# Performance work log

Measured on AMD Instinct MI355X. Metric: run time of the kernel, lower is better.

## Reference

```python
import jax, jax.numpy as jnp
import numpy as np

R, MAXI, MAXO = 333, 119, 12   # n ROIs, max roi input size, max roi reduced size
E, H = 3328, 8                  # embed dim (concat 3325 + pad 3), heads
HD = E // H                     # 416
CONCAT = 3325
EPS = 1e-5


def _roi_layout():
    """Deterministic synthetic ROI sizes + gather maps for vectorized ragged encode."""
    sizes = 30 + (7 * np.arange(R)) % 90            # per-ROI input widths
    reduced = 8 + np.arange(R) % 5                  # per-ROI output widths
    reduced[332] = 8                                # makes concat+3 divisible by 8
    starts = np.concatenate([[0], np.cumsum(sizes)[:-1]])
    total = int(sizes.sum())                        # 24696
    in_idx = np.minimum(starts[:, None] + np.arange(MAXI)[None, :], total - 1)
    in_mask = (np.arange(MAXI)[None, :] < sizes[:, None]).astype(np.float32)
    out_idx = np.concatenate([i * MAXO + np.arange(reduced[i]) for i in range(R)])
    assert out_idx.shape[0] == CONCAT
    return jnp.asarray(in_idx), jnp.asarray(in_mask), jnp.asarray(out_idx)


def _bn(x, g, b):
    # training-mode BatchNorm1d: biased batch stats (matches torch normalization)
    m = x.mean(0)
    v = x.var(0)
    return (x - m) * jax.lax.rsqrt(v + EPS) * g + b


def _lrelu(x, s):
    return jnp.where(x > 0, x, s * x)


def setup_inputs() -> dict:
    key = jax.random.key(0)
    ks = jax.random.split(key, 16)
    B, TOTAL = 2048, 24696
    f32 = jnp.float32
    return {
        'x': jax.random.normal(ks[0], (B, TOTAL), f32),
        'enc_W': jax.random.normal(ks[1], (R, MAXO, MAXI), f32) * 0.1,
        'enc_b': jax.random.normal(ks[2], (R, MAXO), f32) * 0.02,
        'bn1_g': jnp.ones((CONCAT,), f32),
        'bn1_b': jnp.zeros((CONCAT,), f32),
        'Wqkv': jax.random.normal(ks[3], (3 * E, E), f32) * (1.0 / np.sqrt(E)),
        'bqkv': jnp.zeros((3 * E,), f32),
        'Wo': jax.random.normal(ks[4], (E, E), f32) * (1.0 / np.sqrt(E)),
        'bo': jnp.zeros((E,), f32),
        'W1': jax.random.normal(ks[5], (1024, E), f32) * (1.0 / np.sqrt(E)),
        'b1': jnp.zeros((1024,), f32),
        'bn2_g': jnp.ones((1024,), f32),
        'bn2_b': jnp.zeros((1024,), f32),
        'W2': jax.random.normal(ks[6], (300, 1024), f32) * (1.0 / 32.0),
        'b2': jnp.zeros((300,), f32),
        'Wc': jax.random.normal(ks[7], (180, 300), f32) * 0.06,
        'bc': jnp.zeros((180,), f32),
    }


def reference(x, enc_W, enc_b, bn1_g, bn1_b, Wqkv, bqkv, Wo, bo,
              W1, b1, bn2_g, bn2_b, W2, b2, Wc, bc):
    in_idx, in_mask, out_idx = _roi_layout()
    B = x.shape[0]
    # --- vectorized ragged per-ROI Linear (replaces 333-way python loop) ---
    xp = x[:, in_idx] * in_mask                     # [B, R, MAXI], padded slices
    y = jnp.einsum('bri,roi->bro', xp, enc_W) + enc_b  # [B, R, MAXO]
    y = y.reshape(B, R * MAXO)[:, out_idx]          # ragged concat -> [B, 3325]
    # per-ROI BN+LeakyReLU(0.3) == per-feature on the concat
    y = _lrelu(_bn(y, bn1_g, bn1_b), 0.3)
    y = jnp.pad(y, ((0, 0), (1, 2)))                # F.pad (1, 2) -> [B, 3328]
    # --- MultiheadAttention, seq_len = 1 (input unsqueezed to [1, B, E]) ---
    qkv = y @ Wqkv.T + bqkv                         # [B, 3E]
    q, k, v = jnp.split(qkv, 3, axis=-1)
    q = q.reshape(B, H, 1, HD)
    k = k.reshape(B, H, 1, HD)
    v = v.reshape(B, H, 1, HD)
    s = jnp.einsum('bhqd,bhkd->bhqk', q, k) / jnp.sqrt(jnp.float32(HD))
    a = jax.nn.softmax(s, axis=-1)                  # trivially 1 for L=1, kept faithful
    o = jnp.einsum('bhqk,bhkd->bhqd', a, v).reshape(B, E)
    o = o @ Wo.T + bo
    r = _lrelu(_bn(o @ W1.T + b1, bn2_g, bn2_b), 0.1)
    reg_out = r @ W2.T + b2                         # [B, 300]
    y_pred = jax.nn.softmax(reg_out @ Wc.T + bc, axis=-1)  # [B, 180]
    return reg_out, y_pred
```

## Files before the change

kernel.cpp:

```cpp
#include <hip/hip_runtime.h>
#include <hip/hip_bf16.h>

#define B_      2048
#define R_      333
#define MAXI_   119
#define MAXO_   12
#define CONCAT_ 3325
#define E_      3328
#define TOTAL_  24696
#define HID_    1024
#define NREG_   300
#define NCLS_   180
#define EPS_    1e-5f
#define NS2_    128

typedef __attribute__((ext_vector_type(8))) short bf16x8;
typedef __attribute__((ext_vector_type(4))) float f32x4;

static __device__ inline unsigned short f2bf_rne(float f) {
  unsigned u;
  __builtin_memcpy(&u, &f, 4);
  u += 0x7fff + ((u >> 16) & 1);
  return (unsigned short)(u >> 16);
}
static __device__ inline float bf2f(unsigned short s) {
  unsigned u = (unsigned)s << 16;
  float f;
  __builtin_memcpy(&f, &u, 4);
  return f;
}

__global__ void layout_kernel(int* __restrict__ starts, int* __restrict__ red_starts) {
  if (threadIdx.x == 0 && blockIdx.x == 0) {
    int s = 0, rs = 0;
    for (int r = 0; r < R_; ++r) {
      starts[r] = s;
      red_starts[r] = rs;
      s += 30 + (7 * r) % 90;
      rs += (r == 332) ? 8 : (8 + r % 5);
    }
  }
}

__device__ __forceinline__ void rowdot_body(
    const float* __restrict__ A, const float* __restrict__ v, const float* __restrict__ b,
    float* __restrict__ out, int N, int K, int jb) {
  int wid = threadIdx.x >> 6, lane = threadIdx.x & 63;
  int j = jb * 4 + wid;
  if (j >= N) return;
  const float* row = A + (size_t)j * K;
  float s = 0.f;
  for (int k = lane; k < K; k += 64) s = fmaf(row[k], v[k], s);
  for (int o = 32; o; o >>= 1) s += __shfl_down(s, o);
  if (lane == 0) out[j] = s + b[j];
}

__device__ __forceinline__ void pack_w_body(const float* __restrict__ enc_W,
                                            const int* __restrict__ starts,
                                            unsigned short* __restrict__ Wpk, int r) {
  int tid = threadIdx.x;
  int kc = tid >> 6, lane = tid & 63;
  int size = 30 + (7 * r) % 90;
  int s8 = starts[r] & 7;
  int oc = lane & 15;
  int k0 = kc * 32 + (lane >> 4) * 8;
  unsigned short o[8];
#pragma unroll
  for (int e = 0; e < 8; ++e) {
    int k = k0 + e - s8;
    float v = 0.f;
    if (oc < MAXO_ && k >= 0 && k < size) v = enc_W[((size_t)r * MAXO_ + oc) * MAXI_ + k];
    o[e] = f2bf_rne(v);
  }
  unsigned short* dst = Wpk + ((size_t)r * 4 + kc) * 512 + lane * 8;
  *(ushort4*)dst = *(ushort4*)&o[0];
  *(ushort4*)(dst + 4) = *(ushort4*)&o[4];
}

#define NTR_    ((E_ / 64) * (E_ / 64))
#define NC4A_   (HID_ * E_ / 4)
#define NC4B_   (NREG_ * HID_ / 4)
#define NCAST_  ((NC4A_ + NC4B_ + 255) / 256)
__global__ __launch_bounds__(256) void prep_kernel(
    const float* __restrict__ Wo, const float* __restrict__ Wv,
    unsigned short* __restrict__ WoT, unsigned short* __restrict__ WvT,
    const float* __restrict__ W1, unsigned short* __restrict__ W1b,
    const float* __restrict__ W2, unsigned short* __restrict__ W2b,
    const float* __restrict__ bv, const float* __restrict__ bo, float* __restrict__ t1v,
    const float* __restrict__ enc_W, const int* __restrict__ starts,
    unsigned short* __restrict__ Wpk) {
  __shared__ float tile[64][65];
  int bid = blockIdx.x;
  if (bid < 2 * NTR_) {
    int z = bid / NTR_, rem = bid % NTR_;
    const float* in = z ? Wv : Wo;
    unsigned short* out = z ? WvT : WoT;
    int c0 = (rem % 52) * 64, r0 = (rem / 52) * 64;
    int t = threadIdx.x;
    int ci = t & 63, ri0 = t >> 6;
    for (int ri = ri0; ri < 64; ri += 4)
      tile[ri][ci] = in[(size_t)(r0 + ri) * E_ + c0 + ci];
    __syncthreads();
    int rj = t & 63, i0 = t >> 6;
    for (int i = i0; i < 64; i += 4)
      out[(size_t)(c0 + i) * E_ + r0 + rj] = f2bf_rne(tile[rj][i]);
  } else if (bid < 2 * NTR_ + NCAST_) {
    int i = (bid - 2 * NTR_) * 256 + threadIdx.x;
    const float* src; unsigned short* dst; int idx;
    if (i < NC4A_) { src = W1; dst = W1b; idx = i; }
    else if (i < NC4A_ + NC4B_) { src = W2; dst = W2b; idx = i - NC4A_; }
    else return;
    float4 v = ((const float4*)src)[idx];
    ushort4 o;
    o.x = f2bf_rne(v.x); o.y = f2bf_rne(v.y); o.z = f2bf_rne(v.z); o.w = f2bf_rne(v.w);
    ((ushort4*)dst)[idx] = o;
  } else if (bid < 2 * NTR_ + NCAST_ + E_ / 4) {
    rowdot_body(Wo, bv, bo, t1v, E_, E_, bid - 2 * NTR_ - NCAST_);
  } else {
    pack_w_body(enc_W, starts, Wpk, bid - 2 * NTR_ - NCAST_ - E_ / 4);
  }
}

__device__ __forceinline__ void encode_body(
    const float* __restrict__ x, const unsigned short* __restrict__ Wpk,
    const float* __restrict__ enc_b, const int* __restrict__ starts,
    const int* __restrict__ red_starts,
    unsigned short* __restrict__ yT, int r, int bg) {
  int tid = threadIdx.x;
  int wid = tid >> 6, lane = tid & 63;
  int lr = lane & 15, kg = lane >> 4;

  int size = 30 + (7 * r) % 90;
  int red  = (r == 332) ? 8 : (8 + r % 5);
  int st   = starts[r];
  int s8   = st & 7;
  int a0   = st & ~7;
  int rs   = red_starts[r];
  int nkc  = (s8 + size + 31) >> 5;
  int kmax = TOTAL_ - a0;

  bf16x8 wf[4];
  const unsigned short* wp = Wpk + (size_t)r * 2048 + lane * 8;
#pragma unroll
  for (int kc = 0; kc < 4; ++kc) wf[kc] = *(const bf16x8*)(wp + kc * 512);

  float bofs[4];
#pragma unroll
  for (int reg = 0; reg < 4; ++reg) {
    int oc = kg * 4 + reg;
    bofs[reg] = (oc < MAXO_) ? enc_b[r * MAXO_ + oc] : 0.f;
  }

  for (int t = 0; t < 4; ++t) {
    int b0 = bg * 256 + wid * 64 + t * 16;
    const float* xrow = x + (size_t)(b0 + lr) * TOTAL_ + a0;
    f32x4 acc = {0.f, 0.f, 0.f, 0.f};
#pragma unroll
    for (int kc = 0; kc < 4; ++kc) {
      if (kc < nkc) {
        int k0 = kc * 32 + kg * 8;
        if (k0 + 8 > kmax) k0 = kmax - 8;
        float4 v0 = *(const float4*)(xrow + k0);
        float4 v1 = *(const float4*)(xrow + k0 + 4);
        bf16x8 xf;
        xf[0] = (short)f2bf_rne(v0.x); xf[1] = (short)f2bf_rne(v0.y);
        xf[2] = (short)f2bf_rne(v0.z); xf[3] = (short)f2bf_rne(v0.w);
        xf[4] = (short)f2bf_rne(v1.x); xf[5] = (short)f2bf_rne(v1.y);
        xf[6] = (short)f2bf_rne(v1.z); xf[7] = (short)f2bf_rne(v1.w);
        acc = __builtin_amdgcn_mfma_f32_16x16x32_bf16(wf[kc], xf, acc, 0, 0, 0);
      }
    }
#pragma unroll
    for (int reg = 0; reg < 4; ++reg) {
      int oc = kg * 4 + reg;
      if (oc < red)
        yT[(size_t)(rs + oc) * B_ + b0 + lr] = f2bf_rne(acc[reg] + bofs[reg]);
    }
  }
}

template <int KS, bool OUT_BF16>
__device__ __forceinline__ void gemm_body(
    const unsigned short* __restrict__ A, const unsigned short* __restrict__ W,
    float* __restrict__ Cf, unsigned short* __restrict__ Cb,
    int M, int N, int K, int bx, int by, int bz, unsigned short* smem) {
  unsigned short* a_lds = smem;
  unsigned short* b_lds = smem + 8192;
  int tid = threadIdx.x;
  int wid = tid >> 6, lane = tid & 63;
  int wr = wid >> 1, wc = wid & 1;
  int row0 = by * 128, col0 = bx * 128;
  int lr = lane & 15, kg = lane >> 4;
  int Klocal = K / KS;
  int kbase = bz * Klocal;

  int srow = tid >> 2, sk = (tid & 3) * 8;
  const unsigned short* aptr0 = A + (size_t)(row0 + srow) * K + kbase + sk;
  const unsigned short* aptr1 = aptr0 + (size_t)64 * K;
  int bcol0 = col0 + srow;      if (bcol0 > N - 1) bcol0 = N - 1;
  int bcol1 = col0 + 64 + srow; if (bcol1 > N - 1) bcol1 = N - 1;
  const unsigned short* bptr0 = W + (size_t)bcol0 * K + kbase + sk;
  const unsigned short* bptr1 = W + (size_t)bcol1 * K + kbase + sk;

  f32x4 acc[4][4] = {};
  int nk = Klocal >> 5;

#define STAGE_(buf, kc)                                                                             \
  do {                                                                                              \
    __builtin_amdgcn_global_load_lds((const __attribute__((address_space(1))) void*)(aptr0 + (kc)), \
        (__attribute__((address_space(3))) void*)(a_lds + (buf) * 4096 + wid * 512), 16, 0, 0);     \
    __builtin_amdgcn_global_load_lds((const __attribute__((address_space(1))) void*)(aptr1 + (kc)), \
        (__attribute__((address_space(3))) void*)(a_lds + (buf) * 4096 + 2048 + wid * 512), 16, 0, 0); \
    __builtin_amdgcn_global_load_lds((const __attribute__((address_space(1))) void*)(bptr0 + (kc)), \
        (__attribute__((address_space(3))) void*)(b_lds + (buf) * 4096 + wid * 512), 16, 0, 0);     \
    __builtin_amdgcn_global_load_lds((const __attribute__((address_space(1))) void*)(bptr1 + (kc)), \
        (__attribute__((address_space(3))) void*)(b_lds + (buf) * 4096 + 2048 + wid * 512), 16, 0, 0); \
  } while (0)

  STAGE_(0, 0);
  __syncthreads();
  int cur = 0;
  for (int t = 0; t < nk; ++t) {
    if (t + 1 < nk) STAGE_(cur ^ 1, (t + 1) * 32);
    bf16x8 a[4], b[4];
#pragma unroll
    for (int f = 0; f < 4; ++f) {
      a[f] = *(const bf16x8*)(a_lds + cur * 4096 + (wr * 64 + f * 16 + lr) * 32 + kg * 8);
      b[f] = *(const bf16x8*)(b_lds + cur * 4096 + (wc * 64 + f * 16 + lr) * 32 + kg * 8);
    }
#pragma unroll
    for (int i = 0; i < 4; ++i)
#pragma unroll
      for (int j = 0; j < 4; ++j)
        acc[i][j] = __builtin_amdgcn_mfma_f32_16x16x32_bf16(a[i], b[j], acc[i][j], 0, 0, 0);
    __syncthreads();
    cur ^= 1;
  }
#undef STAGE_

#pragma unroll
  for (int j = 0; j < 4; ++j) {
    int ccol = col0 + wc * 64 + j * 16 + lr;
    if (ccol >= N) continue;
#pragma unroll
    for (int i = 0; i < 4; ++i) {
#pragma unroll
      for (int reg = 0; reg < 4; ++reg) {
        int crow = row0 + wr * 64 + i * 16 + kg * 4 + reg;
        float v = acc[i][j][reg];
        if (KS == 1) {
          if (OUT_BF16) Cb[(size_t)crow * N + ccol] = f2bf_rne(v);
          else          Cf[(size_t)crow * N + ccol] = v;
        } else {
          Cf[((size_t)bz * M + crow) * N + ccol] = v;
        }
      }
    }
  }
}

#define WA_NB_  ((E_ / 128) * (HID_ / 128))
#define ENC_NB_ (R_ * 8)
__global__ __launch_bounds__(256) void mega_kernel(
    const float* __restrict__ x, const unsigned short* __restrict__ Wpk,
    const float* __restrict__ enc_b, const int* __restrict__ starts,
    const int* __restrict__ red_starts, unsigned short* __restrict__ yT,
    const unsigned short* __restrict__ W1b, const unsigned short* __restrict__ WoT,
    unsigned short* __restrict__ Wa_bf,
    const float* __restrict__ W1, const float* __restrict__ t1v,
    const float* __restrict__ b1, float* __restrict__ zbv) {
  __shared__ __align__(16) unsigned short smem[16384];
  int bid = blockIdx.x;
  if (bid < WA_NB_) {
    gemm_body<1, true>(W1b, WoT, nullptr, Wa_bf, HID_, E_, E_,
                       bid % (E_ / 128), bid / (E_ / 128), 0, smem);
  } else if (bid < WA_NB_ + ENC_NB_) {
    int eb = bid - WA_NB_;
    encode_body(x, Wpk, enc_b, starts, red_starts, yT, eb >> 3, eb & 7);
  } else {
    rowdot_body(W1, t1v, b1, zbv, HID_, E_, bid - WA_NB_ - ENC_NB_);
  }
}

#define WB2_NB_ (WA_NB_ * 2)
#define ST_NB_  ((CONCAT_ + 15) / 16)
__global__ __launch_bounds__(256) void wb_stats_kernel(
    const unsigned short* __restrict__ Wa_bf, const unsigned short* __restrict__ WvT,
    float* __restrict__ Cpart,
    const unsigned short* __restrict__ yT, float* __restrict__ mean, float* __restrict__ rstd) {
  __shared__ __align__(16) unsigned short smem[16384];
  int bid = blockIdx.x;
  if (bid < WB2_NB_) {
    int z = bid / WA_NB_, rem = bid % WA_NB_;
    gemm_body<2, false>(Wa_bf, WvT, Cpart, nullptr, HID_, E_, E_,
                        rem % (E_ / 128), rem / (E_ / 128), z, smem);
  } else {
    int tb = bid - WB2_NB_;
    int t = threadIdx.x;
    int f = tb * 16 + (t >> 4);
    int j = t & 15;
    if (f >= CONCAT_) return;
    const unsigned short* p = yT + (size_t)f * B_ + j * 128;
    float s = 0.f, s2 = 0.f;
#pragma unroll
    for (int i = 0; i < 16; ++i) {
      bf16x8 v = *(const bf16x8*)(p + i * 8);
#pragma unroll
      for (int e = 0; e < 8; ++e) {
        float xv = bf2f((unsigned short)v[e]);
        s += xv; s2 = fmaf(xv, xv, s2);
      }
    }
#pragma unroll
    for (int m = 1; m <= 8; m <<= 1) { s += __shfl_xor(s, m); s2 += __shfl_xor(s2, m); }
    if (j == 0) {
      float mm = s / B_;
      float var = s2 / B_ - mm * mm;
      mean[f] = mm;
      rstd[f] = rsqrtf(var + EPS_);
    }
  }
}

#define TR_NB_ ((E_ / 64) * (B_ / 64))
#define CWB_NB_ (HID_ * E_ / 4 / 256)
__global__ __launch_bounds__(256) void trans_comb_kernel(
    const unsigned short* __restrict__ yT, const float* __restrict__ mean,
    const float* __restrict__ rstd, const float* __restrict__ g,
    const float* __restrict__ bb, unsigned short* __restrict__ Y,
    const float* __restrict__ Cpart, unsigned short* __restrict__ Wb_bf) {
  __shared__ float tile[64][65];
  int bid = blockIdx.x;
  if (bid < TR_NB_) {
    int cc0 = (bid % 52) * 64, b0 = (bid / 52) * 64;
    int t = threadIdx.x;
    int bi = t & 63, ci0 = t >> 6;
    for (int ci = ci0; ci < 64; ci += 4) {
      int c = cc0 + ci - 1;
      float v = 0.f;
      if (c >= 0 && c < CONCAT_) {
        float f = bf2f(yT[(size_t)c * B_ + b0 + bi]);
        v = (f - mean[c]) * rstd[c] * g[c] + bb[c];
        v = v > 0.f ? v : 0.3f * v;
      }
      tile[ci][bi] = v;
    }
    __syncthreads();
    int cj = t & 63, bj0 = t >> 6;
    for (int bj = bj0; bj < 64; bj += 4)
      Y[(size_t)(b0 + bj) * E_ + cc0 + cj] = f2bf_rne(tile[cj][bj]);
  } else {
    int i4 = (bid - TR_NB_) * 256 + threadIdx.x;
    const int MN4 = HID_ * E_ / 4;
    if (i4 >= MN4) return;
    float4 a = ((const float4*)Cpart)[i4];
    float4 b = ((const float4*)(Cpart + (size_t)HID_ * E_))[i4];
    ushort4 o;
    o.x = f2bf_rne(a.x + b.x); o.y = f2bf_rne(a.y + b.y);
    o.z = f2bf_rne(a.z + b.z); o.w = f2bf_rne(a.w + b.w);
    ((ushort4*)Wb_bf)[i4] = o;
  }
}

template <int KS, bool OUT_BF16>
__global__ __launch_bounds__(256) void gemm_kernel(
    const unsigned short* __restrict__ A, const unsigned short* __restrict__ W,
    float* __restrict__ Cf, unsigned short* __restrict__ Cb, int M, int N, int K) {
  __shared__ __align__(16) unsigned short smem[16384];
  gemm_body<KS, OUT_BF16>(A, W, Cf, Cb, M, N, K, blockIdx.x, blockIdx.y, blockIdx.z, smem);
}

__global__ __launch_bounds__(256) void combZ_stats_kernel(
    const float* __restrict__ Cpart, const float* __restrict__ zb,
    float* __restrict__ Z, float* __restrict__ pS, float* __restrict__ pS2) {
  int c = blockIdx.x * 256 + threadIdx.x;
  int ry = blockIdx.y;
  float zbc = zb[c];
  float s1 = 0.f, s2 = 0.f;
  for (int r = ry * 16; r < ry * 16 + 16; ++r) {
    float v = zbc;
#pragma unroll
    for (int z = 0; z < 4; ++z) v += Cpart[((size_t)z * B_ + r) * HID_ + c];
    Z[(size_t)r * HID_ + c] = v;
    s1 += v; s2 = fmaf(v, v, s2);
  }
  pS[ry * HID_ + c] = s1;
  pS2[ry * HID_ + c] = s2;
}

__global__ __launch_bounds__(256) void colstats_final_kernel(
    const float* __restrict__ pS, const float* __restrict__ pS2,
    float* __restrict__ mean, float* __restrict__ rstd) {
  int c = blockIdx.x * 256 + threadIdx.x;
  if (c >= HID_) return;
  float s = 0.f, s2 = 0.f;
  for (int i = 0; i < NS2_; ++i) { s += pS[i * HID_ + c]; s2 += pS2[i * HID_ + c]; }
  float m = s / B_;
  float v = s2 / B_ - m * m;
  mean[c] = m;
  rstd[c] = rsqrtf(v + EPS_);
}

__global__ __launch_bounds__(256) void bn2_apply_kernel(
    const float* __restrict__ Z, const float* __restrict__ mean, const float* __restrict__ rstd,
    const float* __restrict__ g, const float* __restrict__ bb, unsigned short* __restrict__ R) {
  int i = blockIdx.x * 256 + threadIdx.x;
  int c = i & (HID_ - 1);
  float v = (Z[i] - mean[c]) * rstd[c] * g[c] + bb[c];
  v = v > 0.f ? v : 0.1f * v;
  R[i] = f2bf_rne(v);
}

__global__ __launch_bounds__(256) void classifier_kernel(
    const float* __restrict__ Cpart, const float* __restrict__ b2,
    const float* __restrict__ Wc, const float* __restrict__ bc,
    float* __restrict__ reg_out, float* __restrict__ ypred) {
  int b = blockIdx.x;
  __shared__ __align__(16) float rrow[NREG_];
  __shared__ float sl[256];
  int tid = threadIdx.x;
  for (int i = tid; i < NREG_; i += 256) {
    float s = b2[i];
#pragma unroll
    for (int z = 0; z < 4; ++z) s += Cpart[((size_t)z * B_ + b) * NREG_ + i];
    rrow[i] = s;
    reg_out[(size_t)b * NREG_ + i] = s;
  }
  __syncthreads();
  float s = -1e30f;
  if (tid < NCLS_) {
    const float* w = Wc + (size_t)tid * NREG_;
    float acc = 0.f;
    for (int k = 0; k < NREG_; k += 4) {
      float4 wv = *(const float4*)(w + k);
      float4 rv = *(const float4*)(&rrow[k]);
      acc = fmaf(wv.x, rv.x, acc); acc = fmaf(wv.y, rv.y, acc);
      acc = fmaf(wv.z, rv.z, acc); acc = fmaf(wv.w, rv.w, acc);
    }
    s = acc + bc[tid];
  }
  sl[tid] = s;
  __syncthreads();
  for (int o = 128; o > 0; o >>= 1) {
    if (tid < o) sl[tid] = fmaxf(sl[tid], sl[tid + o]);
    __syncthreads();
  }
  float mx = sl[0];
  __syncthreads();
  float e = (tid < NCLS_) ? __expf(s - mx) : 0.f;
  sl[tid] = e;
  __syncthreads();
  for (int o = 128; o > 0; o >>= 1) {
    if (tid < o) sl[tid] += sl[tid + o];
    __syncthreads();
  }
  if (tid < NCLS_) ypred[(size_t)b * NCLS_ + tid] = e / sl[0];
}

extern "C" void kernel_launch(void* const* d_in, const int* in_sizes, int n_in,
                              void* d_out, int out_size, void* d_ws, size_t ws_size,
                              hipStream_t stream) {
  const float* x     = (const float*)d_in[0];
  const float* enc_W = (const float*)d_in[1];
  const float* enc_b = (const float*)d_in[2];
  const float* bn1_g = (const float*)d_in[3];
  const float* bn1_b = (const float*)d_in[4];
  const float* Wqkv  = (const float*)d_in[5];
  const float* bqkv  = (const float*)d_in[6];
  const float* Wo    = (const float*)d_in[7];
  const float* bo    = (const float*)d_in[8];
  const float* W1    = (const float*)d_in[9];
  const float* b1    = (const float*)d_in[10];
  const float* bn2_g = (const float*)d_in[11];
  const float* bn2_b = (const float*)d_in[12];
  const float* W2    = (const float*)d_in[13];
  const float* b2    = (const float*)d_in[14];
  const float* Wc    = (const float*)d_in[15];
  const float* bc    = (const float*)d_in[16];

  char* ws = (char*)d_ws;
  size_t off = 0;
  auto alloc = [&](size_t bytes) -> void* {
    void* p = ws + off;
    off += (bytes + 255) & ~(size_t)255;
    return p;
  };

  unsigned short* yT     = (unsigned short*)alloc((size_t)CONCAT_ * B_ * 2);
  float*          mean1  = (float*)alloc(CONCAT_ * 4);
  float*          rstd1  = (float*)alloc(CONCAT_ * 4);
  unsigned short* Ybf    = (unsigned short*)alloc((size_t)B_ * E_ * 2);
  unsigned short* Rbf    = (unsigned short*)alloc((size_t)B_ * HID_ * 2);
  unsigned short* WoT_bf = (unsigned short*)alloc((size_t)E_ * E_ * 2);
  unsigned short* WvT_bf = (unsigned short*)alloc((size_t)E_ * E_ * 2);
  unsigned short* W1_bf  = (unsigned short*)alloc((size_t)HID_ * E_ * 2);
  unsigned short* W2_bf  = (unsigned short*)alloc((size_t)NREG_ * HID_ * 2);
  unsigned short* Wa_bf  = (unsigned short*)alloc((size_t)HID_ * E_ * 2);
  unsigned short* Wb_bf  = (unsigned short*)alloc((size_t)HID_ * E_ * 2);
  unsigned short* Wpk    = (unsigned short*)alloc((size_t)R_ * 2048 * 2);
  float*          Cpart  = (float*)alloc((size_t)4 * B_ * HID_ * 4);
  float*          t1v    = (float*)alloc(E_ * 4);
  float*          zbv    = (float*)alloc(HID_ * 4);
  float*          partS  = (float*)alloc((size_t)NS2_ * HID_ * 4);
  float*          partS2 = (float*)alloc((size_t)NS2_ * HID_ * 4);
  float*          mean2  = (float*)alloc(HID_ * 4);
  float*          rstd2  = (float*)alloc(HID_ * 4);
  int*            starts = (int*)alloc(R_ * 4);
  int*            redst  = (int*)alloc(R_ * 4);

  float* Z = (float*)yT;

  layout_kernel<<<1, 1, 0, stream>>>(starts, redst);
  prep_kernel<<<2 * NTR_ + NCAST_ + E_ / 4 + R_, 256, 0, stream>>>(
      Wo, Wqkv + (size_t)2 * E_ * E_, WoT_bf, WvT_bf,
      W1, W1_bf, W2, W2_bf, bqkv + 2 * E_, bo, t1v, enc_W, starts, Wpk);
  mega_kernel<<<WA_NB_ + ENC_NB_ + HID_ / 4, 256, 0, stream>>>(
      x, Wpk, enc_b, starts, redst, yT, W1_bf, WoT_bf, Wa_bf, W1, t1v, b1, zbv);
  wb_stats_kernel<<<WB2_NB_ + ST_NB_, 256, 0, stream>>>(
      Wa_bf, WvT_bf, Cpart, yT, mean1, rstd1);
  trans_comb_kernel<<<TR_NB_ + CWB_NB_, 256, 0, stream>>>(
      yT, mean1, rstd1, bn1_g, bn1_b, Ybf, Cpart, Wb_bf);
  gemm_kernel<4, false><<<dim3(HID_ / 128, B_ / 128, 4), 256, 0, stream>>>(
      Ybf, Wb_bf, Cpart, nullptr, B_, HID_, E_);
  combZ_stats_kernel<<<dim3(HID_ / 256, NS2_), 256, 0, stream>>>(Cpart, zbv, Z, partS, partS2);
  colstats_final_kernel<<<(HID_ + 255) / 256, 256, 0, stream>>>(partS, partS2, mean2, rstd2);
  bn2_apply_kernel<<<(B_ * HID_) / 256, 256, 0, stream>>>(Z, mean2, rstd2, bn2_g, bn2_b, Rbf);
  gemm_kernel<4, false><<<dim3((NREG_ + 127) / 128, B_ / 128, 4), 256, 0, stream>>>(
      Rbf, W2_bf, Cpart, nullptr, B_, NREG_, HID_);
  float* reg_out = (float*)d_out;
  classifier_kernel<<<B_, 256, 0, stream>>>(
      Cpart, b2, Wc, bc, reg_out, reg_out + (size_t)B_ * NREG_);
}
```

Baseline: 313.6 us.

## Split encode across two fused launches to balance GEMM and encode work

The ROI encode is split so that each block handles 64 batch rows instead of 256, with twice the block count. Half of the encode blocks run alongside the Wa GEMM in the first fused kernel and the other half alongside the Wb GEMM in the second. BN1 stats then move to a kernel with the Wb combine, and the BN1 transpose becomes its own kernel. This is meant to balance memory-bound encode with compute-bound GEMM blocks across launches, at the cost of one extra kernel launch.

```diff
diff --git a/kernel.cpp b/kernel.cpp
--- a/kernel.cpp
+++ b/kernel.cpp
@@ -151,31 +151,29 @@
     bofs[reg] = (oc < MAXO_) ? enc_b[r * MAXO_ + oc] : 0.f;
   }
 
-  for (int t = 0; t < 4; ++t) {
-    int b0 = bg * 256 + wid * 64 + t * 16;
-    const float* xrow = x + (size_t)(b0 + lr) * TOTAL_ + a0;
-    f32x4 acc = {0.f, 0.f, 0.f, 0.f};
-#pragma unroll
-    for (int kc = 0; kc < 4; ++kc) {
-      if (kc < nkc) {
-        int k0 = kc * 32 + kg * 8;
-        if (k0 + 8 > kmax) k0 = kmax - 8;
-        float4 v0 = *(const float4*)(xrow + k0);
-        float4 v1 = *(const float4*)(xrow + k0 + 4);
-        bf16x8 xf;
-        xf[0] = (short)f2bf_rne(v0.x); xf[1] = (short)f2bf_rne(v0.y);
-        xf[2] = (short)f2bf_rne(v0.z); xf[3] = (short)f2bf_rne(v0.w);
-        xf[4] = (short)f2bf_rne(v1.x); xf[5] = (short)f2bf_rne(v1.y);
-        xf[6] = (short)f2bf_rne(v1.z); xf[7] = (short)f2bf_rne(v1.w);
-        acc = __builtin_amdgcn_mfma_f32_16x16x32_bf16(wf[kc], xf, acc, 0, 0, 0);
-      }
-    }
-#pragma unroll
-    for (int reg = 0; reg < 4; ++reg) {
-      int oc = kg * 4 + reg;
-      if (oc < red)
-        yT[(size_t)(rs + oc) * B_ + b0 + lr] = f2bf_rne(acc[reg] + bofs[reg]);
-    }
+  int b0 = bg * 64 + wid * 16;
+  const float* xrow = x + (size_t)(b0 + lr) * TOTAL_ + a0;
+  f32x4 acc = {0.f, 0.f, 0.f, 0.f};
+#pragma unroll
+  for (int kc = 0; kc < 4; ++kc) {
+    if (kc < nkc) {
+      int k0 = kc * 32 + kg * 8;
+      if (k0 + 8 > kmax) k0 = kmax - 8;
+      float4 v0 = *(const float4*)(xrow + k0);
+      float4 v1 = *(const float4*)(xrow + k0 + 4);
+      bf16x8 xf;
+      xf[0] = (short)f2bf_rne(v0.x); xf[1] = (short)f2bf_rne(v0.y);
+      xf[2] = (short)f2bf_rne(v0.z); xf[3] = (short)f2bf_rne(v0.w);
+      xf[4] = (short)f2bf_rne(v1.x); xf[5] = (short)f2bf_rne(v1.y);
+      xf[6] = (short)f2bf_rne(v1.z); xf[7] = (short)f2bf_rne(v1.w);
+      acc = __builtin_amdgcn_mfma_f32_16x16x32_bf16(wf[kc], xf, acc, 0, 0, 0);
+    }
+  }
+#pragma unroll
+  for (int reg = 0; reg < 4; ++reg) {
+    int oc = kg * 4 + reg;
+    if (oc < red)
+      yT[(size_t)(rs + oc) * B_ + b0 + lr] = f2bf_rne(acc[reg] + bofs[reg]);
   }
 }
 
@@ -259,9 +257,9 @@
   }
 }
 
-#define WA_NB_  ((E_ / 128) * (HID_ / 128))
-#define ENC_NB_ (R_ * 8)
-__global__ __launch_bounds__(256) void mega_kernel(
+#define WA_NB_   ((E_ / 128) * (HID_ / 128))
+#define ENCH_NB_ (R_ * 16)
+__global__ __launch_bounds__(256) void mega_a_kernel(
     const float* __restrict__ x, const unsigned short* __restrict__ Wpk,
     const float* __restrict__ enc_b, const int* __restrict__ starts,
     const int* __restrict__ red_starts, unsigned short* __restrict__ yT,
@@ -274,20 +272,21 @@
   if (bid < WA_NB_) {
     gemm_body<1, true>(W1b, WoT, nullptr, Wa_bf, HID_, E_, E_,
                        bid % (E_ / 128), bid / (E_ / 128), 0, smem);
-  } else if (bid < WA_NB_ + ENC_NB_) {
+  } else if (bid < WA_NB_ + ENCH_NB_) {
     int eb = bid - WA_NB_;
-    encode_body(x, Wpk, enc_b, starts, red_starts, yT, eb >> 3, eb & 7);
+    encode_body(x, Wpk, enc_b, starts, red_starts, yT, eb >> 4, eb & 15);
   } else {
-    rowdot_body(W1, t1v, b1, zbv, HID_, E_, bid - WA_NB_ - ENC_NB_);
+    rowdot_body(W1, t1v, b1, zbv, HID_, E_, bid - WA_NB_ - ENCH_NB_);
   }
 }
 
 #define WB2_NB_ (WA_NB_ * 2)
-#define ST_NB_  ((CONCAT_ + 15) / 16)
-__global__ __launch_bounds__(256) void wb_stats_kernel(
+__global__ __launch_bounds__(256) void mega_b_kernel(
+    const float* __restrict__ x, const unsigned short* __restrict__ Wpk,
+    const float* __restrict__ enc_b, const int* __restrict__ starts,
+    const int* __restrict__ red_starts, unsigned short* __restrict__ yT,
     const unsigned short* __restrict__ Wa_bf, const unsigned short* __restrict__ WvT,
-    float* __restrict__ Cpart,
-    const unsigned short* __restrict__ yT, float* __restrict__ mean, float* __restrict__ rstd) {
+    float* __restrict__ Cpart) {
   __shared__ __align__(16) unsigned short smem[16384];
   int bid = blockIdx.x;
   if (bid < WB2_NB_) {
@@ -295,9 +294,20 @@
     gemm_body<2, false>(Wa_bf, WvT, Cpart, nullptr, HID_, E_, E_,
                         rem % (E_ / 128), rem / (E_ / 128), z, smem);
   } else {
-    int tb = bid - WB2_NB_;
+    int eb = bid - WB2_NB_;
+    encode_body(x, Wpk, enc_b, starts, red_starts, yT, eb >> 4, 16 + (eb & 15));
+  }
+}
+
+#define ST_NB_  ((CONCAT_ + 15) / 16)
+#define CWB_NB_ (HID_ * E_ / 4 / 256)
+__global__ __launch_bounds__(256) void stats_comb_kernel(
+    const unsigned short* __restrict__ yT, float* __restrict__ mean, float* __restrict__ rstd,
+    const float* __restrict__ Cpart, unsigned short* __restrict__ Wb_bf) {
+  int bid = blockIdx.x;
+  if (bid < ST_NB_) {
     int t = threadIdx.x;
-    int f = tb * 16 + (t >> 4);
+    int f = bid * 16 + (t >> 4);
     int j = t & 15;
     if (f >= CONCAT_) return;
     const unsigned short* p = yT + (size_t)f * B_ + j * 128;
@@ -319,38 +329,8 @@
       mean[f] = mm;
       rstd[f] = rsqrtf(var + EPS_);
     }
-  }
-}
-
-#define TR_NB_ ((E_ / 64) * (B_ / 64))
-#define CWB_NB_ (HID_ * E_ / 4 / 256)
-__global__ __launch_bounds__(256) void trans_comb_kernel(
-    const unsigned short* __restrict__ yT, const float* __restrict__ mean,
-    const float* __restrict__ rstd, const float* __restrict__ g,
-    const float* __restrict__ bb, unsigned short* __restrict__ Y,
-    const float* __restrict__ Cpart, unsigned short* __restrict__ Wb_bf) {
-  __shared__ float tile[64][65];
-  int bid = blockIdx.x;
-  if (bid < TR_NB_) {
-    int cc0 = (bid % 52) * 64, b0 = (bid / 52) * 64;
-    int t = threadIdx.x;
-    int bi = t & 63, ci0 = t >> 6;
-    for (int ci = ci0; ci < 64; ci += 4) {
-      int c = cc0 + ci - 1;
-      float v = 0.f;
-      if (c >= 0 && c < CONCAT_) {
-        float f = bf2f(yT[(size_t)c * B_ + b0 + bi]);
-        v = (f - mean[c]) * rstd[c] * g[c] + bb[c];
-        v = v > 0.f ? v : 0.3f * v;
-      }
-      tile[ci][bi] = v;
-    }
-    __syncthreads();
-    int cj = t & 63, bj0 = t >> 6;
-    for (int bj = bj0; bj < 64; bj += 4)
-      Y[(size_t)(b0 + bj) * E_ + cc0 + cj] = f2bf_rne(tile[cj][bj]);
   } else {
-    int i4 = (bid - TR_NB_) * 256 + threadIdx.x;
+    int i4 = (bid - ST_NB_) * 256 + threadIdx.x;
     const int MN4 = HID_ * E_ / 4;
     if (i4 >= MN4) return;
     float4 a = ((const float4*)Cpart)[i4];
@@ -360,6 +340,32 @@
     o.z = f2bf_rne(a.z + b.z); o.w = f2bf_rne(a.w + b.w);
     ((ushort4*)Wb_bf)[i4] = o;
   }
+}
+
+#define TR_NB_ ((E_ / 64) * (B_ / 64))
+__global__ __launch_bounds__(256) void bn1_transpose_kernel(
+    const unsigned short* __restrict__ yT, const float* __restrict__ mean,
+    const float* __restrict__ rstd, const float* __restrict__ g,
+    const float* __restrict__ bb, unsigned short* __restrict__ Y) {
+  __shared__ float tile[64][65];
+  int bid = blockIdx.x;
+  int cc0 = (bid % 52) * 64, b0 = (bid / 52) * 64;
+  int t = threadIdx.x;
+  int bi = t & 63, ci0 = t >> 6;
+  for (int ci = ci0; ci < 64; ci += 4) {
+    int c = cc0 + ci - 1;
+    float v = 0.f;
+    if (c >= 0 && c < CONCAT_) {
+      float f = bf2f(yT[(size_t)c * B_ + b0 + bi]);
+      v = (f - mean[c]) * rstd[c] * g[c] + bb[c];
+      v = v > 0.f ? v : 0.3f * v;
+    }
+    tile[ci][bi] = v;
+  }
+  __syncthreads();
+  int cj = t & 63, bj0 = t >> 6;
+  for (int bj = bj0; bj < 64; bj += 4)
+    Y[(size_t)(b0 + bj) * E_ + cc0 + cj] = f2bf_rne(tile[cj][bj]);
 }
 
 template <int KS, bool OUT_BF16>
@@ -514,12 +520,14 @@
   prep_kernel<<<2 * NTR_ + NCAST_ + E_ / 4 + R_, 256, 0, stream>>>(
       Wo, Wqkv + (size_t)2 * E_ * E_, WoT_bf, WvT_bf,
       W1, W1_bf, W2, W2_bf, bqkv + 2 * E_, bo, t1v, enc_W, starts, Wpk);
-  mega_kernel<<<WA_NB_ + ENC_NB_ + HID_ / 4, 256, 0, stream>>>(
+  mega_a_kernel<<<WA_NB_ + ENCH_NB_ + HID_ / 4, 256, 0, stream>>>(
       x, Wpk, enc_b, starts, redst, yT, W1_bf, WoT_bf, Wa_bf, W1, t1v, b1, zbv);
-  wb_stats_kernel<<<WB2_NB_ + ST_NB_, 256, 0, stream>>>(
-      Wa_bf, WvT_bf, Cpart, yT, mean1, rstd1);
-  trans_comb_kernel<<<TR_NB_ + CWB_NB_, 256, 0, stream>>>(
-      yT, mean1, rstd1, bn1_g, bn1_b, Ybf, Cpart, Wb_bf);
+  mega_b_kernel<<<WB2_NB_ + ENCH_NB_, 256, 0, stream>>>(
+      x, Wpk, enc_b, starts, redst, yT, Wa_bf, WvT_bf, Cpart);
+  stats_comb_kernel<<<ST_NB_ + CWB_NB_, 256, 0, stream>>>(
+      yT, mean1, rstd1, Cpart, Wb_bf);
+  bn1_transpose_kernel<<<TR_NB_, 256, 0, stream>>>(
+      yT, mean1, rstd1, bn1_g, bn1_b, Ybf);
   gemm_kernel<4, false><<<dim3(HID_ / 128, B_ / 128, 4), 256, 0, stream>>>(
       Ybf, Wb_bf, Cpart, nullptr, B_, HID_, E_);
   combZ_stats_kernel<<<dim3(HID_ / 256, NS2_), 256, 0, stream>>>(Cpart, zbv, Z, partS, partS2);
```

New measurement: 312.7 us, median of 2. About the same (-0.3%).
